# Optimization experiments

Hardware: AMD Instinct MI355X
Metric: run time of the kernel (lower is better)

## Reference

```python
import jax, jax.numpy as jnp
import numpy as np

N_TAPS = 2
N_DELAY = 1
N_ITER = 3
EPS_MODEL = 1e-5   # LaplaceModel clamp eps (eps_models['laplace'])
EPS = 1e-3         # ISS divide/clamp eps


def mag_sq(x):
    return jnp.real(x) ** 2 + jnp.imag(x) ** 2


def laplace_weights(X):
    # Laplace source model: w[..., c, n] = 1 / (2 * ||X[..., c, :, n]||_2), broadcast over freq
    # X: (..., c, f, n) complex -> weights: (..., c, 1, n) real
    denom = 2.0 * jnp.sqrt(jnp.sum(mag_sq(X), axis=-2, keepdims=True))
    return 1.0 / jnp.maximum(denom, EPS_MODEL)


def iss_type1(src, Xc, weights):
    # Equation (9): update vector for source `src`
    Xs = Xc[..., src, :, :]  # (..., f, n)
    v_num = jnp.mean(weights * Xc * jnp.conj(Xs)[..., None, :, :], axis=-1)  # (..., c, f)
    v_denom = jnp.mean(weights * mag_sq(Xs)[..., None, :, :], axis=-1)       # (..., c, f) real
    v = v_num / jnp.maximum(v_denom, EPS)
    v_s = 1.0 - 1.0 / jnp.sqrt(jnp.maximum(v_denom[..., src, :], EPS))
    v = v.at[..., src, :].set(v_s.astype(v.dtype))
    return v


def iss_type2(src, tap, Xc, X_bar, weights):
    # update vector for dereverberation tap (src, tap)
    Xst = X_bar[..., src, :, tap, :]  # (..., f, n)
    v_num = jnp.mean(weights * Xc * jnp.conj(Xst)[..., None, :, :], axis=-1)
    # NOTE: the source code does NOT apply the 1/n_frames norm to v_denom here
    v_denom = jnp.sum(weights * mag_sq(Xst)[..., None, :, :], axis=-1)
    return v_num / jnp.maximum(v_denom, EPS)


def epoch_update(Xloc, Xc, W, X_bar, n_chan):
    weights = laplace_weights(Xloc)  # (..., c, 1, n)
    g = jnp.maximum(jnp.mean(mag_sq(Xloc), axis=(-2, -1), keepdims=True), 1e-5)
    Xloc = Xloc / jnp.sqrt(g)
    weights = weights * g
    for src in range(n_chan):
        v = iss_type1(src, Xc, weights)  # (..., c, f)
        Xc = Xc - v[..., None] * Xc[..., src, :, :][..., None, :, :]
        W = W - v[..., None] * W[..., src, :, :][..., None, :, :]
    for src in range(n_chan):
        for tap in range(N_TAPS):
            v = iss_type2(src, tap, Xc, X_bar, weights)
            Xc = Xc - v[..., None] * X_bar[..., src, :, tap, :][..., None, :, :]
    return Xloc, Xc, W


def auxiva_t_iss(X):
    batch = X.shape[:-3]
    n_chan, n_freq, n_frames = X.shape[-3:]
    T, D = N_TAPS, N_DELAY
    # hankel view of left-padded signal; keep only the T oldest rows (delayed taps)
    X_pad = jnp.pad(X, [(0, 0)] * (X.ndim - 1) + [(T + D, 0)])
    # X_bar: (..., c, f, T, n), X_bar[..., tap, t] = X[..., t - (T + D) + tap]
    X_bar = jnp.stack([X_pad[..., t:t + n_frames] for t in range(T)], axis=-2)
    eye = jnp.eye(n_chan, dtype=X.dtype)
    W = jnp.broadcast_to(eye[:, None, :], batch + (n_chan, n_freq, n_chan))
    Xloc = X  # the (buggy-but-faithful) local X that only gets renormalized each epoch
    Xc = X    # self.X, the demixed signal updated by ISS
    for _ in range(N_ITER):
        Xloc, Xc, W = epoch_update(Xloc, Xc, W, X_bar, n_chan)
    # projection back: a_f = (W_f^T)^{-1} e1 per frequency
    WT = jnp.swapaxes(jnp.swapaxes(W, -3, -2), -2, -1)  # (..., f, c, c)
    e1 = jnp.zeros((n_chan, 1), dtype=X.dtype).at[0, 0].set(1.0)
    a = jnp.linalg.solve(WT, e1)       # (..., f, c, 1)
    a = jnp.swapaxes(a, -3, -2)        # (..., c, f, 1)
    return Xc * a


def setup_inputs() -> dict:
    key = jax.random.key(0)
    k1, k2 = jax.random.split(key)
    shape = (4, 4, 257, 1024)  # (batch, n_chan, n_freq, n_frames)
    X_real = jax.random.normal(k1, shape, dtype=jnp.float32)
    X_imag = jax.random.normal(k2, shape, dtype=jnp.float32)
    return {"X_real": X_real, "X_imag": X_imag}


def reference(X_real, X_imag):
    X = jax.lax.complex(X_real, X_imag)
    return auxiva_t_iss(X)
```

## Files before the change

kernel.cpp:

```cpp
#include <hip/hip_runtime.h>
#include <math.h>

#define NB 4
#define NC 4
#define NF 257
#define NFR 1024
#define NTOT (NB * NC * NF * NFR)
#define NBC (NB * NC)
#define EPSV 1e-3f
#define EPS_MODEL 1e-5f
#define NCHUNK 32

typedef float v2f __attribute__((ext_vector_type(2)));

__device__ float g_Spart[NCHUNK * NBC * NFR];
__device__ float g_S[NBC * NFR];
__device__ float g_gP[96];

__device__ __forceinline__ float dpp_red_sum(float v) {
  v += __int_as_float(__builtin_amdgcn_update_dpp(0, __float_as_int(v), 0x111, 0xf, 0xf, true));
  v += __int_as_float(__builtin_amdgcn_update_dpp(0, __float_as_int(v), 0x112, 0xf, 0xf, true));
  v += __int_as_float(__builtin_amdgcn_update_dpp(0, __float_as_int(v), 0x114, 0xf, 0xf, true));
  v += __int_as_float(__builtin_amdgcn_update_dpp(0, __float_as_int(v), 0x118, 0xf, 0xf, true));
  v += __int_as_float(__builtin_amdgcn_update_dpp(0, __float_as_int(v), 0x142, 0xa, 0xf, true));
  v += __int_as_float(__builtin_amdgcn_update_dpp(0, __float_as_int(v), 0x143, 0xc, 0xf, true));
  return v;
}

__global__ __launch_bounds__(256) void k_colsum(const float* __restrict__ Xr,
                                                const float* __restrict__ Xi) {
  int u = blockIdx.x * 256 + threadIdx.x;
  int fc = blockIdx.y;
  int f0 = fc * 9;
  int f1 = f0 + 9; if (f1 > NF) f1 = NF;
  int bc = u >> 8, q = u & 255;
  float4 s = make_float4(0.f, 0.f, 0.f, 0.f);
  for (int f = f0; f < f1; ++f) {
    float4 a = reinterpret_cast<const float4*>(Xr + (bc * NF + f) * NFR)[q];
    float4 b = reinterpret_cast<const float4*>(Xi + (bc * NF + f) * NFR)[q];
    s.x += a.x * a.x + b.x * b.x;
    s.y += a.y * a.y + b.y * b.y;
    s.z += a.z * a.z + b.z * b.z;
    s.w += a.w * a.w + b.w * b.w;
  }
  reinterpret_cast<float4*>(g_Spart + fc * (NBC * NFR) + bc * NFR)[q] = s;
}

__global__ __launch_bounds__(256) void k_redgp() {
  int bc = blockIdx.x, tid = threadIdx.x;
  float4 s = make_float4(0.f, 0.f, 0.f, 0.f);
#pragma unroll
  for (int fc = 0; fc < NCHUNK; ++fc) {
    float4 a = reinterpret_cast<const float4*>(g_Spart + fc * (NBC * NFR) + bc * NFR)[tid];
    s.x += a.x; s.y += a.y; s.z += a.z; s.w += a.w;
  }
  reinterpret_cast<float4*>(g_S + bc * NFR)[tid] = s;
  float p = dpp_red_sum(s.x + s.y + s.z + s.w);
  __shared__ float r[4];
  if ((tid & 63) == 63) r[tid >> 6] = p;
  __syncthreads();
  if (tid == 0) {
    float s0 = (r[0] + r[1] + r[2] + r[3]) / (float)(NF * NFR);
    float P = 1.f;
#pragma unroll
    for (int e = 0; e < 3; ++e) {
      float g = fmaxf(s0 / P, 1e-5f);
      g_gP[e * 32 + bc] = g;
      g_gP[e * 32 + 16 + bc] = P;
      P *= g;
    }
  }
}

__device__ __forceinline__ void block_reduce12(float* __restrict__ p,
                                               float (*red)[4][12], int buf,
                                               int lane, int wvid,
                                               float* __restrict__ s) {
#pragma unroll
  for (int k = 0; k < 12; ++k) p[k] = dpp_red_sum(p[k]);
  if (lane == 63) {
    float4* dst = reinterpret_cast<float4*>(&red[buf][wvid][0]);
    dst[0] = make_float4(p[0], p[1], p[2], p[3]);
    dst[1] = make_float4(p[4], p[5], p[6], p[7]);
    dst[2] = make_float4(p[8], p[9], p[10], p[11]);
  }
  __syncthreads();
  const float4* r = reinterpret_cast<const float4*>(&red[buf][0][0]);
#pragma unroll
  for (int k = 0; k < 3; ++k) {
    float4 a = r[k], b = r[3 + k], c = r[6 + k], d = r[9 + k];
    s[4 * k + 0] = a.x + b.x + c.x + d.x;
    s[4 * k + 1] = a.y + b.y + c.y + d.y;
    s[4 * k + 2] = a.z + b.z + c.z + d.z;
    s[4 * k + 3] = a.w + b.w + c.w + d.w;
  }
}

__global__ __launch_bounds__(256, 2) void k_main(const float* __restrict__ Xr,
                                                 const float* __restrict__ Xi,
                                                 float* __restrict__ out, int nout) {
  const int blk = blockIdx.x;
  const int b = blk / NF, f = blk % NF;
  const int tid = threadIdx.x;
  const int lane = tid & 63, wvid = tid >> 6;
  const float invN = 1.f / (float)NFR;

  __shared__ float red[2][4][12];
  __shared__ float Wre[NC][NC], Wim[NC][NC];
  __shared__ float abc[8];

  v2f xcr[NC][2], xci[NC][2];
  int rowbase[NC];
#pragma unroll
  for (int c = 0; c < NC; ++c) {
    rowbase[c] = ((b * NC + c) * NF + f) * NFR;
    const float4* pr = reinterpret_cast<const float4*>(Xr + rowbase[c]);
    const float4* pi = reinterpret_cast<const float4*>(Xi + rowbase[c]);
    float4 a0 = pr[tid];
    float4 b0 = pi[tid];
    xcr[c][0] = (v2f){a0.x, a0.y}; xcr[c][1] = (v2f){a0.z, a0.w};
    xci[c][0] = (v2f){b0.x, b0.y}; xci[c][1] = (v2f){b0.z, b0.w};
  }
  if (tid < 16) {
    Wre[tid >> 2][tid & 3] = ((tid >> 2) == (tid & 3)) ? 1.f : 0.f;
    Wim[tid >> 2][tid & 3] = 0.f;
  }

  v2f w2[NC][2];
  int buf = 0;

  for (int e = 0; e < 3; ++e) {
#pragma unroll
    for (int c = 0; c < NC; ++c) {
      float g = g_gP[e * 32 + b * NC + c];
      float P = g_gP[e * 32 + 16 + b * NC + c];
      float sc = __builtin_amdgcn_rcpf(P);
      const float4* ps = reinterpret_cast<const float4*>(g_S + (b * NC + c) * NFR);
      float4 S0 = ps[tid];
      float sv[4] = {S0.x, S0.y, S0.z, S0.w};
      float wv[4];
#pragma unroll
      for (int j = 0; j < 4; ++j)
        wv[j] = g * __builtin_amdgcn_rcpf(fmaxf(2.f * __builtin_amdgcn_sqrtf(sv[j] * sc), EPS_MODEL));
      w2[c][0] = (v2f){wv[0], wv[1]};
      w2[c][1] = (v2f){wv[2], wv[3]};
    }

    for (int src = 0; src < NC; ++src) {
      v2f p2[12];
#pragma unroll
      for (int k = 0; k < 12; ++k) p2[k] = (v2f){0.f, 0.f};
#pragma unroll
      for (int h = 0; h < 2; ++h) {
        v2f xsr = xcr[src][h], xsi = xci[src][h];
        v2f msq = xsr * xsr + xsi * xsi;
#pragma unroll
        for (int c = 0; c < NC; ++c) {
          v2f wv = w2[c][h];
          p2[c]     += wv * (xcr[c][h] * xsr + xci[c][h] * xsi);
          p2[4 + c] += wv * (xci[c][h] * xsr - xcr[c][h] * xsi);
          p2[8 + c] += wv * msq;
        }
      }
      float p[12];
#pragma unroll
      for (int k = 0; k < 12; ++k) p[k] = p2[k].x + p2[k].y;
      float s12[12];
      block_reduce12(p, red, buf, lane, wvid, s12);
      buf ^= 1;

      float vr[NC], vi[NC];
#pragma unroll
      for (int c = 0; c < NC; ++c) {
        float den = fmaxf(s12[8 + c] * invN, EPSV);
        if (c == src) {
          vr[c] = 1.f - __builtin_amdgcn_rsqf(den);
          vi[c] = 0.f;
        } else {
          float sc = invN * __builtin_amdgcn_rcpf(den);
          vr[c] = s12[c] * sc;
          vi[c] = s12[4 + c] * sc;
        }
      }
#pragma unroll
      for (int h = 0; h < 2; ++h) {
        v2f xsr = xcr[src][h], xsi = xci[src][h];
#pragma unroll
        for (int c = 0; c < NC; ++c) {
          xcr[c][h] -= xsr * vr[c] - xsi * vi[c];
          xci[c][h] -= xsi * vr[c] + xsr * vi[c];
        }
      }
      if (tid == 0) {
#pragma unroll
        for (int jj = 0; jj < NC; ++jj) {
          float wsr = Wre[src][jj], wsi = Wim[src][jj];
#pragma unroll
          for (int c = 0; c < NC; ++c) {
            Wre[c][jj] -= vr[c] * wsr - vi[c] * wsi;
            Wim[c][jj] -= vr[c] * wsi + vi[c] * wsr;
          }
        }
      }
    }

    for (int src = 0; src < NC; ++src) {
      const float4* pr = reinterpret_cast<const float4*>(Xr + rowbase[src]);
      const float4* pi = reinterpret_cast<const float4*>(Xi + rowbase[src]);
      float4 A4r = make_float4(0.f, 0.f, 0.f, 0.f), A4i = A4r;
      if (tid > 0) { A4r = pr[tid - 1]; A4i = pi[tid - 1]; }
      float4 B4r = pr[tid], B4i = pi[tid];
      float wr[5] = {A4r.y, A4r.z, A4r.w, B4r.x, B4r.y};
      float wi[5] = {A4i.y, A4i.z, A4i.w, B4i.x, B4i.y};
#pragma unroll
      for (int tap = 0; tap < 2; ++tap) {
        v2f xs_r[2], xs_i[2];
#pragma unroll
        for (int h = 0; h < 2; ++h) {
          xs_r[h] = (v2f){wr[tap + 2 * h], wr[tap + 2 * h + 1]};
          xs_i[h] = (v2f){wi[tap + 2 * h], wi[tap + 2 * h + 1]};
        }
        v2f p2[12];
#pragma unroll
        for (int k = 0; k < 12; ++k) p2[k] = (v2f){0.f, 0.f};
#pragma unroll
        for (int h = 0; h < 2; ++h) {
          v2f xsr = xs_r[h], xsi = xs_i[h];
          v2f msq = xsr * xsr + xsi * xsi;
#pragma unroll
          for (int c = 0; c < NC; ++c) {
            v2f wv = w2[c][h];
            p2[c]     += wv * (xcr[c][h] * xsr + xci[c][h] * xsi);
            p2[4 + c] += wv * (xci[c][h] * xsr - xcr[c][h] * xsi);
            p2[8 + c] += wv * msq;
          }
        }
        float p[12];
#pragma unroll
        for (int k = 0; k < 12; ++k) p[k] = p2[k].x + p2[k].y;
        float s12[12];
        block_reduce12(p, red, buf, lane, wvid, s12);
        buf ^= 1;

        float vr[NC], vi[NC];
#pragma unroll
        for (int c = 0; c < NC; ++c) {
          float den = fmaxf(s12[8 + c], EPSV);
          float sc = invN * __builtin_amdgcn_rcpf(den);
          vr[c] = s12[c] * sc;
          vi[c] = s12[4 + c] * sc;
        }
#pragma unroll
        for (int h = 0; h < 2; ++h) {
          v2f xsr = xs_r[h], xsi = xs_i[h];
#pragma unroll
          for (int c = 0; c < NC; ++c) {
            xcr[c][h] -= xsr * vr[c] - xsi * vi[c];
            xci[c][h] -= xsi * vr[c] + xsr * vi[c];
          }
        }
      }
    }
  }

  __syncthreads();
  if (tid == 0) {
    float Ar[4][4], Ai[4][4];
    float br[4] = {1.f, 0.f, 0.f, 0.f}, bi[4] = {0.f, 0.f, 0.f, 0.f};
#pragma unroll
    for (int i = 0; i < 4; ++i)
#pragma unroll
      for (int j = 0; j < 4; ++j) {
        Ar[i][j] = Wre[j][i];
        Ai[i][j] = Wim[j][i];
      }
    for (int k = 0; k < 4; ++k) {
      int piv = k;
      float best = Ar[k][k] * Ar[k][k] + Ai[k][k] * Ai[k][k];
      for (int i = k + 1; i < 4; ++i) {
        float m = Ar[i][k] * Ar[i][k] + Ai[i][k] * Ai[i][k];
        if (m > best) { best = m; piv = i; }
      }
      if (piv != k) {
        for (int j = 0; j < 4; ++j) {
          float t = Ar[k][j]; Ar[k][j] = Ar[piv][j]; Ar[piv][j] = t;
          t = Ai[k][j]; Ai[k][j] = Ai[piv][j]; Ai[piv][j] = t;
        }
        float t = br[k]; br[k] = br[piv]; br[piv] = t;
        t = bi[k]; bi[k] = bi[piv]; bi[piv] = t;
      }
      float dr = Ar[k][k], di = Ai[k][k];
      float inv = 1.f / (dr * dr + di * di);
      for (int i = k + 1; i < 4; ++i) {
        float fr = (Ar[i][k] * dr + Ai[i][k] * di) * inv;
        float fi = (Ai[i][k] * dr - Ar[i][k] * di) * inv;
        for (int j = k; j < 4; ++j) {
          Ar[i][j] -= fr * Ar[k][j] - fi * Ai[k][j];
          Ai[i][j] -= fr * Ai[k][j] + fi * Ar[k][j];
        }
        br[i] -= fr * br[k] - fi * bi[k];
        bi[i] -= fr * bi[k] + fi * br[k];
      }
    }
    float ar[4], ai[4];
    for (int k = 3; k >= 0; --k) {
      float sr = br[k], si = bi[k];
      for (int j = k + 1; j < 4; ++j) {
        sr -= Ar[k][j] * ar[j] - Ai[k][j] * ai[j];
        si -= Ar[k][j] * ai[j] + Ai[k][j] * ar[j];
      }
      float dr = Ar[k][k], di = Ai[k][k];
      float inv = 1.f / (dr * dr + di * di);
      ar[k] = (sr * dr + si * di) * inv;
      ai[k] = (si * dr - sr * di) * inv;
    }
#pragma unroll
    for (int c = 0; c < 4; ++c) { abc[c] = ar[c]; abc[4 + c] = ai[c]; }
  }
  __syncthreads();

#pragma unroll
  for (int c = 0; c < NC; ++c) {
    float ar = abc[c], ai2 = abc[4 + c];
    if (rowbase[c] + 4 * tid + 3 < nout) {
      float4* po = reinterpret_cast<float4*>(out + rowbase[c]);
      v2f o0 = xcr[c][0] * ar - xci[c][0] * ai2;
      v2f o1 = xcr[c][1] * ar - xci[c][1] * ai2;
      po[tid] = make_float4(o0.x, o0.y, o1.x, o1.y);
    }
  }
}

extern "C" void kernel_launch(void* const* d_in, const int* in_sizes, int n_in,
                              void* d_out, int out_size, void* d_ws, size_t ws_size,
                              hipStream_t stream) {
  const float* Xr = (const float*)d_in[0];
  const float* Xi = (const float*)d_in[1];
  float* out = (float*)d_out;

  dim3 g1(16, NCHUNK);
  k_colsum<<<g1, 256, 0, stream>>>(Xr, Xi);
  k_redgp<<<16, 256, 0, stream>>>();
  k_main<<<NB * NF, 256, 0, stream>>>(Xr, Xi, out, out_size);
}
```

Baseline: 222.0 us.

## Use one wavefront per frequency block and replace block reductions with wave reductions

Shrinks each k_main block from four wavefronts to one, so each lane now holds 16 frames per channel instead of 4. All ISS reductions become wave-level DPP reductions broadcast with readlane, which removes the shared-memory exchange and the block barrier on every ISS step. To save registers, the per-frame Laplace weights are stored in LDS. The cost is fewer waves per CU and more serial work per lane, so there is less latency hiding.

Measured after the change: 276.6 us. 24.6% more time.

```diff
diff --git a/kernel.cpp b/kernel.cpp
--- a/kernel.cpp
+++ b/kernel.cpp
@@ -25,6 +25,11 @@
   v += __int_as_float(__builtin_amdgcn_update_dpp(0, __float_as_int(v), 0x142, 0xa, 0xf, true));
   v += __int_as_float(__builtin_amdgcn_update_dpp(0, __float_as_int(v), 0x143, 0xc, 0xf, true));
   return v;
+}
+
+__device__ __forceinline__ float wred(float v) {
+  v = dpp_red_sum(v);
+  return __int_as_float(__builtin_amdgcn_readlane(__float_as_int(v), 63));
 }
 
 __global__ __launch_bounds__(256) void k_colsum(const float* __restrict__ Xr,
@@ -72,199 +77,199 @@
   }
 }
 
-__device__ __forceinline__ void block_reduce12(float* __restrict__ p,
-                                               float (*red)[4][12], int buf,
-                                               int lane, int wvid,
-                                               float* __restrict__ s) {
-#pragma unroll
-  for (int k = 0; k < 12; ++k) p[k] = dpp_red_sum(p[k]);
-  if (lane == 63) {
-    float4* dst = reinterpret_cast<float4*>(&red[buf][wvid][0]);
-    dst[0] = make_float4(p[0], p[1], p[2], p[3]);
-    dst[1] = make_float4(p[4], p[5], p[6], p[7]);
-    dst[2] = make_float4(p[8], p[9], p[10], p[11]);
-  }
-  __syncthreads();
-  const float4* r = reinterpret_cast<const float4*>(&red[buf][0][0]);
-#pragma unroll
-  for (int k = 0; k < 3; ++k) {
-    float4 a = r[k], b = r[3 + k], c = r[6 + k], d = r[9 + k];
-    s[4 * k + 0] = a.x + b.x + c.x + d.x;
-    s[4 * k + 1] = a.y + b.y + c.y + d.y;
-    s[4 * k + 2] = a.z + b.z + c.z + d.z;
-    s[4 * k + 3] = a.w + b.w + c.w + d.w;
-  }
-}
-
-__global__ __launch_bounds__(256, 2) void k_main(const float* __restrict__ Xr,
-                                                 const float* __restrict__ Xi,
-                                                 float* __restrict__ out, int nout) {
+template <int SRC>
+__device__ __forceinline__ void t1_sweep(v2f (&xcr)[NC][8], v2f (&xci)[NC][8],
+                                         const v2f* __restrict__ wlds,
+                                         float (&Wre)[NC][NC], float (&Wim)[NC][NC],
+                                         int lane, float invN) {
+  v2f p2[12];
+#pragma unroll
+  for (int k = 0; k < 12; ++k) p2[k] = (v2f){0.f, 0.f};
+#pragma unroll
+  for (int h = 0; h < 8; ++h) {
+    v2f xsr = xcr[SRC][h], xsi = xci[SRC][h];
+    v2f msq = xsr * xsr + xsi * xsi;
+#pragma unroll
+    for (int c = 0; c < NC; ++c) {
+      v2f wv = wlds[(h * 4 + c) * 64 + lane];
+      p2[c]     += wv * (xcr[c][h] * xsr + xci[c][h] * xsi);
+      p2[4 + c] += wv * (xci[c][h] * xsr - xcr[c][h] * xsi);
+      p2[8 + c] += wv * msq;
+    }
+  }
+  float s12[12];
+#pragma unroll
+  for (int k = 0; k < 12; ++k) s12[k] = wred(p2[k].x + p2[k].y);
+
+  float vr[NC], vi[NC];
+#pragma unroll
+  for (int c = 0; c < NC; ++c) {
+    float den = fmaxf(s12[8 + c] * invN, EPSV);
+    if (c == SRC) {
+      vr[c] = 1.f - __builtin_amdgcn_rsqf(den);
+      vi[c] = 0.f;
+    } else {
+      float sc = invN * __builtin_amdgcn_rcpf(den);
+      vr[c] = s12[c] * sc;
+      vi[c] = s12[4 + c] * sc;
+    }
+  }
+#pragma unroll
+  for (int h = 0; h < 8; ++h) {
+    v2f xsr = xcr[SRC][h], xsi = xci[SRC][h];
+#pragma unroll
+    for (int c = 0; c < NC; ++c) {
+      xcr[c][h] -= xsr * vr[c] - xsi * vi[c];
+      xci[c][h] -= xsi * vr[c] + xsr * vi[c];
+    }
+  }
+  if (lane == 0) {
+#pragma unroll
+    for (int jj = 0; jj < NC; ++jj) {
+      float wsr = Wre[SRC][jj], wsi = Wim[SRC][jj];
+#pragma unroll
+      for (int c = 0; c < NC; ++c) {
+        Wre[c][jj] -= vr[c] * wsr - vi[c] * wsi;
+        Wim[c][jj] -= vr[c] * wsi + vi[c] * wsr;
+      }
+    }
+  }
+}
+
+__device__ __forceinline__ void t2_sweep(const float* __restrict__ prb,
+                                         const float* __restrict__ pib,
+                                         v2f (&xcr)[NC][8], v2f (&xci)[NC][8],
+                                         const v2f* __restrict__ wlds,
+                                         int lane, float invN) {
+  const float4* pr = reinterpret_cast<const float4*>(prb);
+  const float4* pi = reinterpret_cast<const float4*>(pib);
+  float4 A4r = make_float4(0.f, 0.f, 0.f, 0.f), A4i = A4r;
+  if (lane > 0) { A4r = pr[4 * lane - 1]; A4i = pi[4 * lane - 1]; }
+  float4 B0r = pr[4 * lane],     B0i = pi[4 * lane];
+  float4 B1r = pr[4 * lane + 1], B1i = pi[4 * lane + 1];
+  float4 B2r = pr[4 * lane + 2], B2i = pi[4 * lane + 2];
+  float4 B3r = pr[4 * lane + 3], B3i = pi[4 * lane + 3];
+  float wr[17] = {A4r.y, A4r.z, A4r.w, B0r.x, B0r.y, B0r.z, B0r.w,
+                  B1r.x, B1r.y, B1r.z, B1r.w, B2r.x, B2r.y, B2r.z, B2r.w,
+                  B3r.x, B3r.y};
+  float wi[17] = {A4i.y, A4i.z, A4i.w, B0i.x, B0i.y, B0i.z, B0i.w,
+                  B1i.x, B1i.y, B1i.z, B1i.w, B2i.x, B2i.y, B2i.z, B2i.w,
+                  B3i.x, B3i.y};
+
+#pragma unroll
+  for (int tap = 0; tap < 2; ++tap) {
+    v2f p2[12];
+#pragma unroll
+    for (int k = 0; k < 12; ++k) p2[k] = (v2f){0.f, 0.f};
+#pragma unroll
+    for (int h = 0; h < 8; ++h) {
+      v2f xsr = (v2f){wr[tap + 2 * h], wr[tap + 2 * h + 1]};
+      v2f xsi = (v2f){wi[tap + 2 * h], wi[tap + 2 * h + 1]};
+      v2f msq = xsr * xsr + xsi * xsi;
+#pragma unroll
+      for (int c = 0; c < NC; ++c) {
+        v2f wv = wlds[(h * 4 + c) * 64 + lane];
+        p2[c]     += wv * (xcr[c][h] * xsr + xci[c][h] * xsi);
+        p2[4 + c] += wv * (xci[c][h] * xsr - xcr[c][h] * xsi);
+        p2[8 + c] += wv * msq;
+      }
+    }
+    float s12[12];
+#pragma unroll
+    for (int k = 0; k < 12; ++k) s12[k] = wred(p2[k].x + p2[k].y);
+
+    float vr[NC], vi[NC];
+#pragma unroll
+    for (int c = 0; c < NC; ++c) {
+      float den = fmaxf(s12[8 + c], EPSV);
+      float sc = invN * __builtin_amdgcn_rcpf(den);
+      vr[c] = s12[c] * sc;
+      vi[c] = s12[4 + c] * sc;
+    }
+#pragma unroll
+    for (int h = 0; h < 8; ++h) {
+      v2f xsr = (v2f){wr[tap + 2 * h], wr[tap + 2 * h + 1]};
+      v2f xsi = (v2f){wi[tap + 2 * h], wi[tap + 2 * h + 1]};
+#pragma unroll
+      for (int c = 0; c < NC; ++c) {
+        xcr[c][h] -= xsr * vr[c] - xsi * vi[c];
+        xci[c][h] -= xsi * vr[c] + xsr * vi[c];
+      }
+    }
+  }
+}
+
+__global__ __launch_bounds__(64, 1) void k_main(const float* __restrict__ Xr,
+                                                const float* __restrict__ Xi,
+                                                float* __restrict__ out, int nout) {
   const int blk = blockIdx.x;
   const int b = blk / NF, f = blk % NF;
-  const int tid = threadIdx.x;
-  const int lane = tid & 63, wvid = tid >> 6;
+  const int lane = threadIdx.x;
   const float invN = 1.f / (float)NFR;
 
-  __shared__ float red[2][4][12];
+  __shared__ v2f wlds[32 * 64];
   __shared__ float Wre[NC][NC], Wim[NC][NC];
   __shared__ float abc[8];
 
-  v2f xcr[NC][2], xci[NC][2];
+  v2f xcr[NC][8], xci[NC][8];
   int rowbase[NC];
 #pragma unroll
   for (int c = 0; c < NC; ++c) {
     rowbase[c] = ((b * NC + c) * NF + f) * NFR;
     const float4* pr = reinterpret_cast<const float4*>(Xr + rowbase[c]);
     const float4* pi = reinterpret_cast<const float4*>(Xi + rowbase[c]);
-    float4 a0 = pr[tid];
-    float4 b0 = pi[tid];
-    xcr[c][0] = (v2f){a0.x, a0.y}; xcr[c][1] = (v2f){a0.z, a0.w};
-    xci[c][0] = (v2f){b0.x, b0.y}; xci[c][1] = (v2f){b0.z, b0.w};
-  }
-  if (tid < 16) {
-    Wre[tid >> 2][tid & 3] = ((tid >> 2) == (tid & 3)) ? 1.f : 0.f;
-    Wim[tid >> 2][tid & 3] = 0.f;
-  }
-
-  v2f w2[NC][2];
-  int buf = 0;
+#pragma unroll
+    for (int k = 0; k < 4; ++k) {
+      float4 a = pr[4 * lane + k];
+      float4 bb = pi[4 * lane + k];
+      xcr[c][2 * k]     = (v2f){a.x, a.y};
+      xcr[c][2 * k + 1] = (v2f){a.z, a.w};
+      xci[c][2 * k]     = (v2f){bb.x, bb.y};
+      xci[c][2 * k + 1] = (v2f){bb.z, bb.w};
+    }
+  }
+  if (lane == 0) {
+#pragma unroll
+    for (int i = 0; i < NC; ++i)
+#pragma unroll
+      for (int j = 0; j < NC; ++j) {
+        Wre[i][j] = (i == j) ? 1.f : 0.f;
+        Wim[i][j] = 0.f;
+      }
+  }
 
   for (int e = 0; e < 3; ++e) {
 #pragma unroll
     for (int c = 0; c < NC; ++c) {
       float g = g_gP[e * 32 + b * NC + c];
       float P = g_gP[e * 32 + 16 + b * NC + c];
-      float sc = __builtin_amdgcn_rcpf(P);
+      float invP = __builtin_amdgcn_rcpf(P);
       const float4* ps = reinterpret_cast<const float4*>(g_S + (b * NC + c) * NFR);
-      float4 S0 = ps[tid];
-      float sv[4] = {S0.x, S0.y, S0.z, S0.w};
-      float wv[4];
-#pragma unroll
-      for (int j = 0; j < 4; ++j)
-        wv[j] = g * __builtin_amdgcn_rcpf(fmaxf(2.f * __builtin_amdgcn_sqrtf(sv[j] * sc), EPS_MODEL));
-      w2[c][0] = (v2f){wv[0], wv[1]};
-      w2[c][1] = (v2f){wv[2], wv[3]};
-    }
-
-    for (int src = 0; src < NC; ++src) {
-      v2f p2[12];
-#pragma unroll
-      for (int k = 0; k < 12; ++k) p2[k] = (v2f){0.f, 0.f};
-#pragma unroll
-      for (int h = 0; h < 2; ++h) {
-        v2f xsr = xcr[src][h], xsi = xci[src][h];
-        v2f msq = xsr * xsr + xsi * xsi;
-#pragma unroll
-        for (int c = 0; c < NC; ++c) {
-          v2f wv = w2[c][h];
-          p2[c]     += wv * (xcr[c][h] * xsr + xci[c][h] * xsi);
-          p2[4 + c] += wv * (xci[c][h] * xsr - xcr[c][h] * xsi);
-          p2[8 + c] += wv * msq;
-        }
-      }
-      float p[12];
-#pragma unroll
-      for (int k = 0; k < 12; ++k) p[k] = p2[k].x + p2[k].y;
-      float s12[12];
-      block_reduce12(p, red, buf, lane, wvid, s12);
-      buf ^= 1;
-
-      float vr[NC], vi[NC];
-#pragma unroll
-      for (int c = 0; c < NC; ++c) {
-        float den = fmaxf(s12[8 + c] * invN, EPSV);
-        if (c == src) {
-          vr[c] = 1.f - __builtin_amdgcn_rsqf(den);
-          vi[c] = 0.f;
-        } else {
-          float sc = invN * __builtin_amdgcn_rcpf(den);
-          vr[c] = s12[c] * sc;
-          vi[c] = s12[4 + c] * sc;
-        }
-      }
-#pragma unroll
-      for (int h = 0; h < 2; ++h) {
-        v2f xsr = xcr[src][h], xsi = xci[src][h];
-#pragma unroll
-        for (int c = 0; c < NC; ++c) {
-          xcr[c][h] -= xsr * vr[c] - xsi * vi[c];
-          xci[c][h] -= xsi * vr[c] + xsr * vi[c];
-        }
-      }
-      if (tid == 0) {
-#pragma unroll
-        for (int jj = 0; jj < NC; ++jj) {
-          float wsr = Wre[src][jj], wsi = Wim[src][jj];
-#pragma unroll
-          for (int c = 0; c < NC; ++c) {
-            Wre[c][jj] -= vr[c] * wsr - vi[c] * wsi;
-            Wim[c][jj] -= vr[c] * wsi + vi[c] * wsr;
-          }
-        }
-      }
-    }
-
-    for (int src = 0; src < NC; ++src) {
-      const float4* pr = reinterpret_cast<const float4*>(Xr + rowbase[src]);
-      const float4* pi = reinterpret_cast<const float4*>(Xi + rowbase[src]);
-      float4 A4r = make_float4(0.f, 0.f, 0.f, 0.f), A4i = A4r;
-      if (tid > 0) { A4r = pr[tid - 1]; A4i = pi[tid - 1]; }
-      float4 B4r = pr[tid], B4i = pi[tid];
-      float wr[5] = {A4r.y, A4r.z, A4r.w, B4r.x, B4r.y};
-      float wi[5] = {A4i.y, A4i.z, A4i.w, B4i.x, B4i.y};
-#pragma unroll
-      for (int tap = 0; tap < 2; ++tap) {
-        v2f xs_r[2], xs_i[2];
-#pragma unroll
-        for (int h = 0; h < 2; ++h) {
-          xs_r[h] = (v2f){wr[tap + 2 * h], wr[tap + 2 * h + 1]};
-          xs_i[h] = (v2f){wi[tap + 2 * h], wi[tap + 2 * h + 1]};
-        }
-        v2f p2[12];
-#pragma unroll
-        for (int k = 0; k < 12; ++k) p2[k] = (v2f){0.f, 0.f};
-#pragma unroll
-        for (int h = 0; h < 2; ++h) {
-          v2f xsr = xs_r[h], xsi = xs_i[h];
-          v2f msq = xsr * xsr + xsi * xsi;
-#pragma unroll
-          for (int c = 0; c < NC; ++c) {
-            v2f wv = w2[c][h];
-            p2[c]     += wv * (xcr[c][h] * xsr + xci[c][h] * xsi);
-            p2[4 + c] += wv * (xci[c][h] * xsr - xcr[c][h] * xsi);
-            p2[8 + c] += wv * msq;
-          }
-        }
-        float p[12];
-#pragma unroll
-        for (int k = 0; k < 12; ++k) p[k] = p2[k].x + p2[k].y;
-        float s12[12];
-        block_reduce12(p, red, buf, lane, wvid, s12);
-        buf ^= 1;
-
-        float vr[NC], vi[NC];
-#pragma unroll
-        for (int c = 0; c < NC; ++c) {
-          float den = fmaxf(s12[8 + c], EPSV);
-          float sc = invN * __builtin_amdgcn_rcpf(den);
-          vr[c] = s12[c] * sc;
-          vi[c] = s12[4 + c] * sc;
-        }
-#pragma unroll
-        for (int h = 0; h < 2; ++h) {
-          v2f xsr = xs_r[h], xsi = xs_i[h];
-#pragma unroll
-          for (int c = 0; c < NC; ++c) {
-            xcr[c][h] -= xsr * vr[c] - xsi * vi[c];
-            xci[c][h] -= xsi * vr[c] + xsr * vi[c];
-          }
-        }
-      }
-    }
-  }
-
-  __syncthreads();
-  if (tid == 0) {
+#pragma unroll
+      for (int k = 0; k < 4; ++k) {
+        float4 s4 = ps[4 * lane + k];
+        float sv[4] = {s4.x, s4.y, s4.z, s4.w};
+        float wv[4];
+#pragma unroll
+        for (int j = 0; j < 4; ++j)
+          wv[j] = g * __builtin_amdgcn_rcpf(fmaxf(2.f * __builtin_amdgcn_sqrtf(sv[j] * invP), EPS_MODEL));
+        wlds[((2 * k) * 4 + c) * 64 + lane]     = (v2f){wv[0], wv[1]};
+        wlds[((2 * k + 1) * 4 + c) * 64 + lane] = (v2f){wv[2], wv[3]};
+      }
+    }
+
+    t1_sweep<0>(xcr, xci, wlds, Wre, Wim, lane, invN);
+    t1_sweep<1>(xcr, xci, wlds, Wre, Wim, lane, invN);
+    t1_sweep<2>(xcr, xci, wlds, Wre, Wim, lane, invN);
+    t1_sweep<3>(xcr, xci, wlds, Wre, Wim, lane, invN);
+
+    t2_sweep(Xr + rowbase[0], Xi + rowbase[0], xcr, xci, wlds, lane, invN);
+    t2_sweep(Xr + rowbase[1], Xi + rowbase[1], xcr, xci, wlds, lane, invN);
+    t2_sweep(Xr + rowbase[2], Xi + rowbase[2], xcr, xci, wlds, lane, invN);
+    t2_sweep(Xr + rowbase[3], Xi + rowbase[3], xcr, xci, wlds, lane, invN);
+  }
+
+  if (lane == 0) {
     float Ar[4][4], Ai[4][4];
     float br[4] = {1.f, 0.f, 0.f, 0.f}, bi[4] = {0.f, 0.f, 0.f, 0.f};
 #pragma unroll
@@ -322,11 +327,14 @@
 #pragma unroll
   for (int c = 0; c < NC; ++c) {
     float ar = abc[c], ai2 = abc[4 + c];
-    if (rowbase[c] + 4 * tid + 3 < nout) {
+    if (rowbase[c] + 16 * lane + 15 < nout) {
       float4* po = reinterpret_cast<float4*>(out + rowbase[c]);
-      v2f o0 = xcr[c][0] * ar - xci[c][0] * ai2;
-      v2f o1 = xcr[c][1] * ar - xci[c][1] * ai2;
-      po[tid] = make_float4(o0.x, o0.y, o1.x, o1.y);
+#pragma unroll
+      for (int k = 0; k < 4; ++k) {
+        v2f o0 = xcr[c][2 * k] * ar - xci[c][2 * k] * ai2;
+        v2f o1 = xcr[c][2 * k + 1] * ar - xci[c][2 * k + 1] * ai2;
+        po[4 * lane + k] = make_float4(o0.x, o0.y, o1.x, o1.y);
+      }
     }
   }
 }
@@ -341,5 +349,5 @@
   dim3 g1(16, NCHUNK);
   k_colsum<<<g1, 256, 0, stream>>>(Xr, Xi);
   k_redgp<<<16, 256, 0, stream>>>();
-  k_main<<<NB * NF, 256, 0, stream>>>(Xr, Xi, out, out_size);
-}
+  k_main<<<NB * NF, 64, 0, stream>>>(Xr, Xi, out, out_size);
+}
```
